# Kernel tuning notes

Hardware: AMD Instinct MI355X
Metric: run time of the kernel (lower is better)

The kernel has to match this reference:

```python
import jax, jax.numpy as jnp
import numpy as np

B, S, H, I, G = 4, 2048, 2048, 8192, 128


def _onebit_quant(w, group_size):
    # Group-wise 1-bit (sign) quantization along the input dim with per-group
    # abs-mean scale, as in BitNet-style OneBitLinear.
    out_f, in_f = w.shape
    wg = w.reshape(out_f, in_f // group_size, group_size)
    scale = jnp.mean(jnp.abs(wg), axis=-1, keepdims=True)  # [out, n_groups, 1]
    wq = jnp.sign(wg) * scale
    return wq.reshape(out_f, in_f)


def setup_inputs() -> dict:
    key = jax.random.key(0)
    k1, k2, k3, k4 = jax.random.split(key, 4)
    return {
        "x": jax.random.normal(k1, (B, S, H), dtype=jnp.float32),
        "w_gate": jax.random.normal(k2, (I, H), dtype=jnp.float32) * 0.02,
        "w_up": jax.random.normal(k3, (I, H), dtype=jnp.float32) * 0.02,
        "w_down": jax.random.normal(k4, (H, I), dtype=jnp.float32) * 0.02,
        "group_size": G,
    }


def reference(x, w_gate, w_up, w_down, group_size):
    wg_q = _onebit_quant(w_gate, group_size)   # [I, H]
    wu_q = _onebit_quant(w_up, group_size)     # [I, H]
    wd_q = _onebit_quant(w_down, group_size)   # [H, I]
    gate = jnp.einsum('bsh,ih->bsi', x, wg_q)  # [B, S, I]
    up = jnp.einsum('bsh,ih->bsi', x, wu_q)    # [B, S, I]
    h = jax.nn.silu(gate) * up                 # [B, S, I]
    return jnp.einsum('bsi,hi->bsh', h, wd_q)  # [B, S, H]
```

## Files before the change

kernel.cpp:

```cpp
#include <hip/hip_runtime.h>
#include <hip/hip_bf16.h>
#include <cstdint>
#include <cstddef>

using bf16 = __hip_bfloat16;

typedef __attribute__((ext_vector_type(8))) short short8;
typedef __attribute__((ext_vector_type(4))) float f32x4;
typedef __attribute__((ext_vector_type(4))) unsigned short us4;

static constexpr int Bb = 4, Ss = 2048, Hh = 2048, Ii = 8192, Gg = 128;
static constexpr int Mm = Bb * Ss;

#define MEMFENCE() asm volatile("" ::: "memory")
#define BARRIER() do { MEMFENCE(); __builtin_amdgcn_s_barrier(); MEMFENCE(); } while (0)

__global__ void quant_onebit(const float* __restrict__ w, bf16* __restrict__ wq,
                             int ngroups) {
  int gid = blockIdx.x * 4 + (threadIdx.x >> 6);
  if (gid >= ngroups) return;
  int lane = threadIdx.x & 63;
  size_t base = (size_t)gid * Gg + (size_t)lane * 2;
  float2 v = *(const float2*)(w + base);
  float s = fabsf(v.x) + fabsf(v.y);
#pragma unroll
  for (int m = 32; m >= 1; m >>= 1) s += __shfl_xor(s, m);
  float scale = s * (1.0f / 128.0f);
  float q0 = (v.x > 0.f) ? scale : ((v.x < 0.f) ? -scale : 0.f);
  float q1 = (v.y > 0.f) ? scale : ((v.y < 0.f) ? -scale : 0.f);
  unsigned int p =
      (unsigned int)__builtin_bit_cast(unsigned short, __float2bfloat16(q0)) |
      ((unsigned int)__builtin_bit_cast(unsigned short, __float2bfloat16(q1)) << 16);
  *(unsigned int*)(wq + base) = p;
}

__global__ void cast_f32_bf16(const float* __restrict__ in, bf16* __restrict__ out,
                              size_t n4) {
  size_t i = (size_t)blockIdx.x * blockDim.x + threadIdx.x;
  if (i >= n4) return;
  float4 v = *(const float4*)(in + i * 4);
  us4 o;
  o.x = __builtin_bit_cast(unsigned short, __float2bfloat16(v.x));
  o.y = __builtin_bit_cast(unsigned short, __float2bfloat16(v.y));
  o.z = __builtin_bit_cast(unsigned short, __float2bfloat16(v.z));
  o.w = __builtin_bit_cast(unsigned short, __float2bfloat16(v.w));
  *(us4*)(out + i * 4) = o;
}

__device__ __forceinline__ void gload16(const bf16* g, char* l) {
  __builtin_amdgcn_global_load_lds(
      (const __attribute__((address_space(1))) void*)g,
      (__attribute__((address_space(3))) void*)l, 16, 0, 0);
}

__device__ __forceinline__ short8 lds_frag(const char* tileBase, int row, int s) {
  int v = (row ^ (row >> 2)) & 3;
  return *(const short8*)(tileBase + row * 64 + (((s ^ v) & 3) << 4));
}

template <bool DUAL>
__global__ __launch_bounds__(512, 2)
void gemm_bt8(const bf16* __restrict__ A,
              const bf16* __restrict__ B0,
              const bf16* __restrict__ B1,
              bf16* __restrict__ OutBf,
              float* __restrict__ OutF,
              int M, int N, int K) {
  constexpr int BM = 256, BN = DUAL ? 128 : 256, BK = 32;
  constexpr int NF = DUAL ? 2 : 4;
  constexpr int BUFB = 32768;
  extern __shared__ char smem[];

  const int tid = threadIdx.x;
  const int wid = tid >> 6;
  const int lane = tid & 63;
  const int wr = wid >> 2;
  const int wc = wid & 3;
  const int lrow = lane & 15;
  const int s = lane >> 4;

  const int nbx = N / BN;
  const int nwg = (int)gridDim.x;
  const int cpx = nwg >> 3;
  const int wg = (int)blockIdx.x;
  const int swz = (wg & 7) * cpx + (wg >> 3);
  const int m0 = (swz / nbx) * BM;
  const int n0 = (swz % nbx) * BN;

  const int NT = K / BK;

  const int srow = tid >> 2;
  const int sv = (srow ^ (srow >> 2)) & 3;
  const int scol = (((tid & 3) ^ sv) & 3) << 3;
  const bf16* pA0 = A + (size_t)(m0 + srow) * K + scol;
  const bf16* pA1 = A + (size_t)(m0 + 128 + srow) * K + scol;
  const bf16* pB0;
  const bf16* pB1;
  if constexpr (DUAL) {
    pB0 = B0 + (size_t)(n0 + srow) * K + scol;
    pB1 = B1 + (size_t)(n0 + srow) * K + scol;
  } else {
    pB0 = B0 + (size_t)(n0 + srow) * K + scol;
    pB1 = B0 + (size_t)(n0 + 128 + srow) * K + scol;
  }
  const int ldsOff = wid * 1024;

  auto stageA = [&](int u) {
    char* base = smem + (size_t)(u & 3) * BUFB;
    gload16(pA0 + u * BK, base + 0 + ldsOff);
    gload16(pA1 + u * BK, base + 8192 + ldsOff);
  };
  auto stageB = [&](int u) {
    char* base = smem + (size_t)(u & 3) * BUFB;
    gload16(pB0 + u * BK, base + 16384 + ldsOff);
    gload16(pB1 + u * BK, base + 24576 + ldsOff);
  };

  const f32x4 vzero = {0.f, 0.f, 0.f, 0.f};
  f32x4 acc0[8][NF];
  f32x4 acc1[DUAL ? 8 : 1][NF];
#pragma unroll
  for (int mf = 0; mf < 8; ++mf)
#pragma unroll
    for (int nf = 0; nf < NF; ++nf) {
      acc0[mf][nf] = vzero;
      if constexpr (DUAL) acc1[mf][nf] = vzero;
    }

  stageA(0); stageB(0);
  stageA(1); stageB(1);
  stageA(2); stageB(2);
  asm volatile("s_waitcnt vmcnt(8)" ::: "memory");
  __builtin_amdgcn_s_barrier();
  MEMFENCE();

  short8 fb0[NF], fb1[DUAL ? NF : 1];

  for (int t = 0; t < NT; ++t) {
    const char* buf = smem + (size_t)(t & 3) * BUFB;
    const char* Ab = buf;
    const char* Bb = buf + 16384;
    short8 fa[4];

#pragma unroll
    for (int i = 0; i < 4; ++i)
      fa[i] = lds_frag(Ab, wr * 128 + i * 16 + lrow, s);
    if constexpr (DUAL) {
#pragma unroll
      for (int nf = 0; nf < 2; ++nf) {
        fb0[nf] = lds_frag(Bb, wc * 32 + nf * 16 + lrow, s);
        fb1[nf] = lds_frag(buf + 24576, wc * 32 + nf * 16 + lrow, s);
      }
    } else {
#pragma unroll
      for (int nf = 0; nf < 4; ++nf)
        fb0[nf] = lds_frag(Bb, wc * 64 + nf * 16 + lrow, s);
    }
    if (t + 3 < NT) stageA(t + 3);
    BARRIER();
    __builtin_amdgcn_s_setprio(1);
#pragma unroll
    for (int i = 0; i < 4; ++i)
#pragma unroll
      for (int nf = 0; nf < NF; ++nf) {
        acc0[i][nf] = __builtin_amdgcn_mfma_f32_16x16x32_bf16(
            fa[i], fb0[nf], acc0[i][nf], 0, 0, 0);
        if constexpr (DUAL)
          acc1[i][nf] = __builtin_amdgcn_mfma_f32_16x16x32_bf16(
              fa[i], fb1[nf], acc1[i][nf], 0, 0, 0);
      }
    __builtin_amdgcn_s_setprio(0);
    BARRIER();

#pragma unroll
    for (int i = 0; i < 4; ++i)
      fa[i] = lds_frag(Ab, wr * 128 + (4 + i) * 16 + lrow, s);
    if (t + 3 < NT) stageB(t + 3);
    BARRIER();
    __builtin_amdgcn_s_setprio(1);
#pragma unroll
    for (int i = 0; i < 4; ++i)
#pragma unroll
      for (int nf = 0; nf < NF; ++nf) {
        acc0[4 + i][nf] = __builtin_amdgcn_mfma_f32_16x16x32_bf16(
            fa[i], fb0[nf], acc0[4 + i][nf], 0, 0, 0);
        if constexpr (DUAL)
          acc1[4 + i][nf] = __builtin_amdgcn_mfma_f32_16x16x32_bf16(
              fa[i], fb1[nf], acc1[4 + i][nf], 0, 0, 0);
      }
    __builtin_amdgcn_s_setprio(0);

    const int r = NT - 1 - t;
    MEMFENCE();
    if (r >= 3)      asm volatile("s_waitcnt vmcnt(8)" ::: "memory");
    else if (r == 2) asm volatile("s_waitcnt vmcnt(4)" ::: "memory");
    else if (r == 1) asm volatile("s_waitcnt vmcnt(0)" ::: "memory");
    __builtin_amdgcn_s_barrier();
    MEMFENCE();
  }

  const int crow0 = (lane >> 4) * 4;
  const int ccol = lane & 15;
#pragma unroll
  for (int mf = 0; mf < 8; ++mf)
#pragma unroll
    for (int nf = 0; nf < NF; ++nf)
#pragma unroll
      for (int j = 0; j < 4; ++j) {
        const int row = m0 + wr * 128 + mf * 16 + crow0 + j;
        if constexpr (DUAL) {
          const int col = n0 + wc * 32 + nf * 16 + ccol;
          float g = acc0[mf][nf][j];
          float u = acc1[mf][nf][j];
          OutBf[(size_t)row * N + col] =
              __float2bfloat16(g / (1.0f + expf(-g)) * u);
        } else {
          const int col = n0 + wc * 64 + nf * 16 + ccol;
          OutF[(size_t)row * N + col] = acc0[mf][nf][j];
        }
      }
}

extern "C" void kernel_launch(void* const* d_in, const int* in_sizes, int n_in,
                              void* d_out, int out_size, void* d_ws, size_t ws_size,
                              hipStream_t stream) {
  const float* x = (const float*)d_in[0];
  const float* wg = (const float*)d_in[1];
  const float* wu = (const float*)d_in[2];
  const float* wd = (const float*)d_in[3];
  float* out = (float*)d_out;

  char* ws = (char*)d_ws;
  bf16* xq = (bf16*)(ws + 0);
  bf16* wgq = (bf16*)(ws + (size_t)33554432);
  bf16* wuq = (bf16*)(ws + (size_t)67108864);
  bf16* hbuf = (bf16*)(ws + (size_t)100663296);
  bf16* wdq = xq;

  auto* kDual = gemm_bt8<true>;
  auto* kSingle = gemm_bt8<false>;
  (void)hipFuncSetAttribute((const void*)kDual,
                            hipFuncAttributeMaxDynamicSharedMemorySize, 131072);
  (void)hipFuncSetAttribute((const void*)kSingle,
                            hipFuncAttributeMaxDynamicSharedMemorySize, 131072);

  const int ngW = (Ii * Hh) / Gg;
  quant_onebit<<<ngW / 4, 256, 0, stream>>>(wg, wgq, ngW);
  quant_onebit<<<ngW / 4, 256, 0, stream>>>(wu, wuq, ngW);

  const size_t n4 = (size_t)Mm * Hh / 4;
  cast_f32_bf16<<<(unsigned)((n4 + 255) / 256), 256, 0, stream>>>(x, xq, n4);

  kDual<<<(Mm / 256) * (Ii / 128), 512, 131072, stream>>>(
      xq, wgq, wuq, hbuf, nullptr, Mm, Ii, Hh);

  quant_onebit<<<ngW / 4, 256, 0, stream>>>(wd, wdq, ngW);

  kSingle<<<(Mm / 256) * (Hh / 256), 512, 131072, stream>>>(
      hbuf, wdq, nullptr, nullptr, out, Mm, Hh, Ii);
}
```

Baseline: 904.4 us.

## Restructure GEMM main loop to double-buffered BK=64 stages with per-half prefetch

```diff
diff --git a/kernel.cpp b/kernel.cpp
--- a/kernel.cpp
+++ b/kernel.cpp
@@ -53,9 +53,8 @@
       (__attribute__((address_space(3))) void*)l, 16, 0, 0);
 }
 
-__device__ __forceinline__ short8 lds_frag(const char* tileBase, int row, int s) {
-  int v = (row ^ (row >> 2)) & 3;
-  return *(const short8*)(tileBase + row * 64 + (((s ^ v) & 3) << 4));
+__device__ __forceinline__ short8 lfrag(const char* part, int row, int s) {
+  return *(const short8*)(part + row * 64 + (((s ^ (row >> 1)) & 3) << 4));
 }
 
 template <bool DUAL>
@@ -66,9 +65,8 @@
               bf16* __restrict__ OutBf,
               float* __restrict__ OutF,
               int M, int N, int K) {
-  constexpr int BM = 256, BN = DUAL ? 128 : 256, BK = 32;
+  constexpr int BM = 256, BN = DUAL ? 128 : 256;
   constexpr int NF = DUAL ? 2 : 4;
-  constexpr int BUFB = 32768;
   extern __shared__ char smem[];
 
   const int tid = threadIdx.x;
@@ -77,7 +75,7 @@
   const int wr = wid >> 2;
   const int wc = wid & 3;
   const int lrow = lane & 15;
-  const int s = lane >> 4;
+  const int ks = lane >> 4;
 
   const int nbx = N / BN;
   const int nwg = (int)gridDim.x;
@@ -87,33 +85,28 @@
   const int m0 = (swz / nbx) * BM;
   const int n0 = (swz % nbx) * BN;
 
-  const int NT = K / BK;
+  const int NT = K / 64;
 
   const int srow = tid >> 2;
-  const int sv = (srow ^ (srow >> 2)) & 3;
-  const int scol = (((tid & 3) ^ sv) & 3) << 3;
-  const bf16* pA0 = A + (size_t)(m0 + srow) * K + scol;
-  const bf16* pA1 = A + (size_t)(m0 + 128 + srow) * K + scol;
-  const bf16* pB0;
-  const bf16* pB1;
-  if constexpr (DUAL) {
-    pB0 = B0 + (size_t)(n0 + srow) * K + scol;
-    pB1 = B1 + (size_t)(n0 + srow) * K + scol;
-  } else {
-    pB0 = B0 + (size_t)(n0 + srow) * K + scol;
-    pB1 = B0 + (size_t)(n0 + 128 + srow) * K + scol;
-  }
-  const int ldsOff = wid * 1024;
-
-  auto stageA = [&](int u) {
-    char* base = smem + (size_t)(u & 3) * BUFB;
-    gload16(pA0 + u * BK, base + 0 + ldsOff);
-    gload16(pA1 + u * BK, base + 8192 + ldsOff);
+  const int slog8 = (((tid & 3) ^ ((tid >> 3) & 3)) << 3);
+  const bf16* pA0 = A + (size_t)(m0 + srow) * K + slog8;
+  const bf16* pA1 = pA0 + (size_t)128 * K;
+  const bf16* pB0 = B0 + (size_t)(n0 + srow) * K + slog8;
+  const bf16* pB1 = DUAL ? (B1 + (size_t)(n0 + srow) * K + slog8)
+                         : (pB0 + (size_t)128 * K);
+  const int dA = wid * 1024;
+
+  auto stageA = [&](int t, int p) {
+    char* b = smem + (size_t)(t & 1) * 65536 + p * 32768;
+    const int koff = t * 64 + p * 32;
+    gload16(pA0 + koff, b + dA);
+    gload16(pA1 + koff, b + 8192 + dA);
   };
-  auto stageB = [&](int u) {
-    char* base = smem + (size_t)(u & 3) * BUFB;
-    gload16(pB0 + u * BK, base + 16384 + ldsOff);
-    gload16(pB1 + u * BK, base + 24576 + ldsOff);
+  auto stageB = [&](int t, int p) {
+    char* b = smem + (size_t)(t & 1) * 65536 + p * 32768 + 16384;
+    const int koff = t * 64 + p * 32;
+    gload16(pB0 + koff, b + dA);
+    gload16(pB1 + koff, b + 8192 + dA);
   };
 
   const f32x4 vzero = {0.f, 0.f, 0.f, 0.f};
@@ -127,76 +120,69 @@
       if constexpr (DUAL) acc1[mf][nf] = vzero;
     }
 
-  stageA(0); stageB(0);
-  stageA(1); stageB(1);
-  stageA(2); stageB(2);
-  asm volatile("s_waitcnt vmcnt(8)" ::: "memory");
-  __builtin_amdgcn_s_barrier();
-  MEMFENCE();
-
-  short8 fb0[NF], fb1[DUAL ? NF : 1];
+  stageA(0, 0); stageB(0, 0);
+  stageA(0, 1); stageB(0, 1);
+
+  short8 fa[4], fb0[NF], fb1[DUAL ? NF : 1];
 
   for (int t = 0; t < NT; ++t) {
-    const char* buf = smem + (size_t)(t & 3) * BUFB;
-    const char* Ab = buf;
-    const char* Bb = buf + 16384;
-    short8 fa[4];
-
-#pragma unroll
-    for (int i = 0; i < 4; ++i)
-      fa[i] = lds_frag(Ab, wr * 128 + i * 16 + lrow, s);
-    if constexpr (DUAL) {
-#pragma unroll
-      for (int nf = 0; nf < 2; ++nf) {
-        fb0[nf] = lds_frag(Bb, wc * 32 + nf * 16 + lrow, s);
-        fb1[nf] = lds_frag(buf + 24576, wc * 32 + nf * 16 + lrow, s);
+    const char* buf = smem + (size_t)(t & 1) * 65536;
+#pragma unroll
+    for (int p = 0; p < 2; ++p) {
+      const char* Ap = buf + p * 32768;
+      const char* Bp = Ap + 16384;
+
+      if (p == 0 || t + 1 < NT)
+        asm volatile("s_waitcnt vmcnt(4)" ::: "memory");
+      else
+        asm volatile("s_waitcnt vmcnt(0)" ::: "memory");
+      BARRIER();
+      if constexpr (DUAL) {
+#pragma unroll
+        for (int nf = 0; nf < 2; ++nf) {
+          fb0[nf] = lfrag(Bp, wc * 32 + nf * 16 + lrow, ks);
+          fb1[nf] = lfrag(Bp + 8192, wc * 32 + nf * 16 + lrow, ks);
+        }
+      } else {
+#pragma unroll
+        for (int nf = 0; nf < 4; ++nf)
+          fb0[nf] = lfrag(Bp, wc * 64 + nf * 16 + lrow, ks);
       }
-    } else {
-#pragma unroll
-      for (int nf = 0; nf < 4; ++nf)
-        fb0[nf] = lds_frag(Bb, wc * 64 + nf * 16 + lrow, s);
+#pragma unroll
+      for (int i = 0; i < 4; ++i)
+        fa[i] = lfrag(Ap, wr * 128 + i * 16 + lrow, ks);
+      if (t + 1 < NT) stageA(t + 1, p);
+      __builtin_amdgcn_s_setprio(1);
+#pragma unroll
+      for (int i = 0; i < 4; ++i)
+#pragma unroll
+        for (int nf = 0; nf < NF; ++nf) {
+          acc0[i][nf] = __builtin_amdgcn_mfma_f32_16x16x32_bf16(
+              fa[i], fb0[nf], acc0[i][nf], 0, 0, 0);
+          if constexpr (DUAL)
+            acc1[i][nf] = __builtin_amdgcn_mfma_f32_16x16x32_bf16(
+                fa[i], fb1[nf], acc1[i][nf], 0, 0, 0);
+        }
+      __builtin_amdgcn_s_setprio(0);
+      BARRIER();
+
+#pragma unroll
+      for (int i = 0; i < 4; ++i)
+        fa[i] = lfrag(Ap, wr * 128 + 64 + i * 16 + lrow, ks);
+      if (t + 1 < NT) stageB(t + 1, p);
+      __builtin_amdgcn_s_setprio(1);
+#pragma unroll
+      for (int i = 0; i < 4; ++i)
+#pragma unroll
+        for (int nf = 0; nf < NF; ++nf) {
+          acc0[4 + i][nf] = __builtin_amdgcn_mfma_f32_16x16x32_bf16(
+              fa[i], fb0[nf], acc0[4 + i][nf], 0, 0, 0);
+          if constexpr (DUAL)
+            acc1[4 + i][nf] = __builtin_amdgcn_mfma_f32_16x16x32_bf16(
+                fa[i], fb1[nf], acc1[4 + i][nf], 0, 0, 0);
+        }
+      __builtin_amdgcn_s_setprio(0);
     }
-    if (t + 3 < NT) stageA(t + 3);
-    BARRIER();
-    __builtin_amdgcn_s_setprio(1);
-#pragma unroll
-    for (int i = 0; i < 4; ++i)
-#pragma unroll
-      for (int nf = 0; nf < NF; ++nf) {
-        acc0[i][nf] = __builtin_amdgcn_mfma_f32_16x16x32_bf16(
-            fa[i], fb0[nf], acc0[i][nf], 0, 0, 0);
-        if constexpr (DUAL)
-          acc1[i][nf] = __builtin_amdgcn_mfma_f32_16x16x32_bf16(
-              fa[i], fb1[nf], acc1[i][nf], 0, 0, 0);
-      }
-    __builtin_amdgcn_s_setprio(0);
-    BARRIER();
-
-#pragma unroll
-    for (int i = 0; i < 4; ++i)
-      fa[i] = lds_frag(Ab, wr * 128 + (4 + i) * 16 + lrow, s);
-    if (t + 3 < NT) stageB(t + 3);
-    BARRIER();
-    __builtin_amdgcn_s_setprio(1);
-#pragma unroll
-    for (int i = 0; i < 4; ++i)
-#pragma unroll
-      for (int nf = 0; nf < NF; ++nf) {
-        acc0[4 + i][nf] = __builtin_amdgcn_mfma_f32_16x16x32_bf16(
-            fa[i], fb0[nf], acc0[4 + i][nf], 0, 0, 0);
-        if constexpr (DUAL)
-          acc1[4 + i][nf] = __builtin_amdgcn_mfma_f32_16x16x32_bf16(
-              fa[i], fb1[nf], acc1[4 + i][nf], 0, 0, 0);
-      }
-    __builtin_amdgcn_s_setprio(0);
-
-    const int r = NT - 1 - t;
-    MEMFENCE();
-    if (r >= 3)      asm volatile("s_waitcnt vmcnt(8)" ::: "memory");
-    else if (r == 2) asm volatile("s_waitcnt vmcnt(4)" ::: "memory");
-    else if (r == 1) asm volatile("s_waitcnt vmcnt(0)" ::: "memory");
-    __builtin_amdgcn_s_barrier();
-    MEMFENCE();
   }
 
   const int crow0 = (lane >> 4) * 4;
```

New measurement: 842.9 us. 6.8% less time.
